# Performance work log

Hardware: AMD Instinct MI355X
Metric: run time of the kernel (lower is better)

## Reference

```python
import jax, jax.numpy as jnp
import numpy as np

SMOOTHING = 0.9  # NEURON_CONFIG['signal_smoothing']
NUM_SOURCE = 16384
NUM_TARGET = 16384
NUM_BRANCHES = 64
BATCH = 32


def setup_inputs() -> dict:
    key = jax.random.key(0)
    k1, k2, k3, k4 = jax.random.split(key, 4)
    spikes = jax.random.normal(k1, (BATCH, NUM_SOURCE), dtype=jnp.float32)
    attenuation = jax.random.uniform(k2, (NUM_SOURCE, NUM_BRANCHES), dtype=jnp.float32)
    target_indices = jax.random.randint(k3, (NUM_SOURCE, NUM_BRANCHES), 0, NUM_TARGET)
    delays = jax.random.randint(k4, (NUM_SOURCE, NUM_BRANCHES), 0, 6)
    return {"spikes": spikes, "attenuation": attenuation,
            "target_indices": target_indices, "delays": delays}


def reference(spikes, attenuation, target_indices, delays):
    # spikes: [B, S]; attenuation/delays/target_indices: [S, Br]
    B = spikes.shape[0]
    num_target = NUM_TARGET
    att = jnp.clip(attenuation, 0.0, 1.0)
    decay = SMOOTHING ** delays.astype(spikes.dtype)          # [S, Br]
    # fused elementwise: signal per (batch, source, branch)
    signals = spikes[:, :, None] * (att * decay)[None, :, :]   # [B, S, Br]
    flat_t = target_indices.reshape(-1)                        # [S*Br]
    flat_s = signals.reshape(B, -1)                            # [B, S*Br]
    out = jnp.zeros((B, num_target), dtype=spikes.dtype)
    out = out.at[jnp.arange(B)[:, None], flat_t[None, :]].add(flat_s)
    return out
```

## Files before the change

kernel.cpp:

```cpp
#include <hip/hip_runtime.h>

#define S_   16384
#define T_   16384
#define B_   32
#define NEDGES (S_ * 64)
#define GP_  512
#define EPG  2048
#define NBKT 256
#define TPB  64
#define CAPT 128
#define OVF_CAP 64

__device__ __forceinline__ float edge_weight(float a, int d) {
  float w = fminf(fmaxf(a, 0.0f), 1.0f);
  float r = (d & 1) ? 0.9f : 1.0f;
  r = (d & 2) ? r * 0.81f   : r;
  r = (d & 4) ? r * 0.6561f : r;
  return w * r;
}

__global__ __launch_bounds__(512) void produce(
    const float* __restrict__ spikes,
    const float* __restrict__ att,
    const int*   __restrict__ tgt,
    const int*   __restrict__ del,
    float*        __restrict__ spikesT,
    int2*         __restrict__ rec,
    unsigned int* __restrict__ ofse) {
  __shared__ float tile[32][33];
  __shared__ int4  sbuf4[EPG / 2];
  __shared__ int   cnt5[NBKT], cur5[NBKT], sofs5[NBKT];
  __shared__ int   wtot[4];
  int2* buf = (int2*)sbuf4;

  const int g   = blockIdx.x;
  const int tid = threadIdx.x;
  if (tid < NBKT) cnt5[tid] = 0;

  const int s0 = g * 32;
  {
    const int x = tid & 31, y = tid >> 5;
    tile[x][y]      = spikes[(size_t)y        * S_ + s0 + x];
    tile[x][y + 16] = spikes[(size_t)(y + 16) * S_ + s0 + x];
  }

  const int e4  = g * 512 + tid;
  int4   t = reinterpret_cast<const int4*>(tgt)[e4];
  float4 a = reinterpret_cast<const float4*>(att)[e4];
  int4   d = reinterpret_cast<const int4*>(del)[e4];
  const int src = e4 >> 4;

  __syncthreads();

  {
    const int b = tid & 31, j = tid >> 5;
    spikesT[(size_t)(s0 + j)      * 32 + b] = tile[j][b];
    spikesT[(size_t)(s0 + j + 16) * 32 + b] = tile[j + 16][b];
  }

  const int bk0 = t.x >> 6, bk1 = t.y >> 6, bk2 = t.z >> 6, bk3 = t.w >> 6;
  __hip_atomic_fetch_add(&cnt5[bk0], 1, __ATOMIC_RELAXED, __HIP_MEMORY_SCOPE_WORKGROUP);
  __hip_atomic_fetch_add(&cnt5[bk1], 1, __ATOMIC_RELAXED, __HIP_MEMORY_SCOPE_WORKGROUP);
  __hip_atomic_fetch_add(&cnt5[bk2], 1, __ATOMIC_RELAXED, __HIP_MEMORY_SCOPE_WORKGROUP);
  __hip_atomic_fetch_add(&cnt5[bk3], 1, __ATOMIC_RELAXED, __HIP_MEMORY_SCOPE_WORKGROUP);
  __syncthreads();

  int v = 0, incl = 0;
  if (tid < NBKT) {
    v = cnt5[tid];
    incl = v;
#pragma unroll
    for (int off = 1; off < 64; off <<= 1) {
      int u = __shfl_up(incl, off);
      if ((tid & 63) >= off) incl += u;
    }
    if ((tid & 63) == 63) wtot[tid >> 6] = incl;
  }
  __syncthreads();
  if (tid < NBKT) {
    int base = 0;
    const int wv = tid >> 6;
    for (int i = 0; i < wv; ++i) base += wtot[i];
    const int start = base + incl - v;
    sofs5[tid] = start;
    cur5[tid]  = start;
  }
  __syncthreads();

#define PUT(BK, TL, AV, DV)                                                   \
  {                                                                           \
    int p = __hip_atomic_fetch_add(&cur5[BK], 1, __ATOMIC_RELAXED,            \
                                   __HIP_MEMORY_SCOPE_WORKGROUP);             \
    buf[p] = make_int2(((TL) << 14) | src,                                    \
                       __float_as_int(edge_weight((AV), (DV))));              \
  }
  PUT(bk0, t.x & 63, a.x, d.x)
  PUT(bk1, t.y & 63, a.y, d.y)
  PUT(bk2, t.z & 63, a.z, d.z)
  PUT(bk3, t.w & 63, a.w, d.w)
#undef PUT
  __syncthreads();

  int4* recO = reinterpret_cast<int4*>(rec) + (size_t)g * (EPG / 2);
  recO[tid]       = sbuf4[tid];
  recO[tid + 512] = sbuf4[tid + 512];
  if (tid < NBKT)
    ofse[(size_t)tid * GP_ + g] =
        ((unsigned)cur5[tid] << 16) | (unsigned)sofs5[tid];
}

__global__ __launch_bounds__(1024) void consume(
    const int2*  __restrict__ rec,
    const unsigned int* __restrict__ ofse,
    const float* __restrict__ spikesT,
    float* __restrict__ out) {
  __shared__ int2  srt[TPB * CAPT];
  __shared__ float otile[TPB][33];
  __shared__ unsigned sse[GP_];
  __shared__ int   cur64[TPB];
  __shared__ int2  ovf[OVF_CAP];
  __shared__ int   ovfn;

  const int k   = blockIdx.x;
  const int tid = threadIdx.x;
  const int b   = tid & 31;
  const int hw  = tid >> 5;

  if (tid < TPB) cur64[tid] = tid * CAPT;
  if (tid == 0)  ovfn = 0;
  if (tid < GP_) sse[tid] = ofse[(size_t)k * GP_ + tid];
  __syncthreads();

  {
    const int grp = tid >> 3;
    const int l8  = tid & 7;
    for (int it = 0; it < 4; ++it) {
      const int g = grp + it * 128;
      const unsigned u = sse[g];
      const int st = (int)(u & 0xFFFF);
      const int n  = (int)(u >> 16) - st;
      const int2* slice = rec + (size_t)g * EPG + st;
      for (int j = l8; j < n; j += 8) {
        int2 r = slice[j];
        const int tl = (r.x >> 14) & 63;
        int p = __hip_atomic_fetch_add(&cur64[tl], 1, __ATOMIC_RELAXED,
                                       __HIP_MEMORY_SCOPE_WORKGROUP);
        if (p < (tl + 1) * CAPT) {
          srt[p] = r;
        } else {
          int q = __hip_atomic_fetch_add(&ovfn, 1, __ATOMIC_RELAXED,
                                         __HIP_MEMORY_SCOPE_WORKGROUP);
          if (q < OVF_CAP) ovf[q] = r;
        }
      }
    }
  }
  __syncthreads();

  float acc0 = 0.f, acc1 = 0.f;
  int e0 = hw * CAPT;
  int e1 = (hw + 32) * CAPT;
  const int e0e = min(cur64[hw],      (hw + 1)  * CAPT);
  const int e1e = min(cur64[hw + 32], (hw + 33) * CAPT);

  for (; e0 + 4 <= e0e && e1 + 4 <= e1e; e0 += 4, e1 += 4) {
    int2 r0 = srt[e0], r1 = srt[e0 + 1], r2 = srt[e0 + 2], r3 = srt[e0 + 3];
    int2 q0 = srt[e1], q1 = srt[e1 + 1], q2 = srt[e1 + 2], q3 = srt[e1 + 3];
    float s0 = spikesT[(size_t)(r0.x & 0x3FFF) * 32 + b];
    float s1 = spikesT[(size_t)(r1.x & 0x3FFF) * 32 + b];
    float s2 = spikesT[(size_t)(r2.x & 0x3FFF) * 32 + b];
    float s3 = spikesT[(size_t)(r3.x & 0x3FFF) * 32 + b];
    float u0 = spikesT[(size_t)(q0.x & 0x3FFF) * 32 + b];
    float u1 = spikesT[(size_t)(q1.x & 0x3FFF) * 32 + b];
    float u2 = spikesT[(size_t)(q2.x & 0x3FFF) * 32 + b];
    float u3 = spikesT[(size_t)(q3.x & 0x3FFF) * 32 + b];
    acc0 = fmaf(__int_as_float(r0.y), s0, acc0);
    acc0 = fmaf(__int_as_float(r1.y), s1, acc0);
    acc0 = fmaf(__int_as_float(r2.y), s2, acc0);
    acc0 = fmaf(__int_as_float(r3.y), s3, acc0);
    acc1 = fmaf(__int_as_float(q0.y), u0, acc1);
    acc1 = fmaf(__int_as_float(q1.y), u1, acc1);
    acc1 = fmaf(__int_as_float(q2.y), u2, acc1);
    acc1 = fmaf(__int_as_float(q3.y), u3, acc1);
  }
  for (; e0 + 4 <= e0e; e0 += 4) {
    int2 r0 = srt[e0], r1 = srt[e0 + 1], r2 = srt[e0 + 2], r3 = srt[e0 + 3];
    float s0 = spikesT[(size_t)(r0.x & 0x3FFF) * 32 + b];
    float s1 = spikesT[(size_t)(r1.x & 0x3FFF) * 32 + b];
    float s2 = spikesT[(size_t)(r2.x & 0x3FFF) * 32 + b];
    float s3 = spikesT[(size_t)(r3.x & 0x3FFF) * 32 + b];
    acc0 = fmaf(__int_as_float(r0.y), s0, acc0);
    acc0 = fmaf(__int_as_float(r1.y), s1, acc0);
    acc0 = fmaf(__int_as_float(r2.y), s2, acc0);
    acc0 = fmaf(__int_as_float(r3.y), s3, acc0);
  }
  for (; e0 < e0e; ++e0) {
    int2 r = srt[e0];
    acc0 = fmaf(__int_as_float(r.y), spikesT[(size_t)(r.x & 0x3FFF) * 32 + b], acc0);
  }
  for (; e1 + 4 <= e1e; e1 += 4) {
    int2 q0 = srt[e1], q1 = srt[e1 + 1], q2 = srt[e1 + 2], q3 = srt[e1 + 3];
    float u0 = spikesT[(size_t)(q0.x & 0x3FFF) * 32 + b];
    float u1 = spikesT[(size_t)(q1.x & 0x3FFF) * 32 + b];
    float u2 = spikesT[(size_t)(q2.x & 0x3FFF) * 32 + b];
    float u3 = spikesT[(size_t)(q3.x & 0x3FFF) * 32 + b];
    acc1 = fmaf(__int_as_float(q0.y), u0, acc1);
    acc1 = fmaf(__int_as_float(q1.y), u1, acc1);
    acc1 = fmaf(__int_as_float(q2.y), u2, acc1);
    acc1 = fmaf(__int_as_float(q3.y), u3, acc1);
  }
  for (; e1 < e1e; ++e1) {
    int2 q = srt[e1];
    acc1 = fmaf(__int_as_float(q.y), spikesT[(size_t)(q.x & 0x3FFF) * 32 + b], acc1);
  }

  const int no = min(ovfn, OVF_CAP);
  for (int j = 0; j < no; ++j) {
    int2 r = ovf[j];
    const int tl = (r.x >> 14) & 63;
    float s = spikesT[(size_t)(r.x & 0x3FFF) * 32 + b];
    float w = __int_as_float(r.y);
    if (tl == hw)      acc0 = fmaf(w, s, acc0);
    if (tl == hw + 32) acc1 = fmaf(w, s, acc1);
  }

  otile[hw][b]      = acc0;
  otile[hw + 32][b] = acc1;
  __syncthreads();
  const int bb = tid >> 5;
  const int cc = (tid & 31) * 2;
  float2 o2 = make_float2(otile[cc][bb], otile[cc + 1][bb]);
  *reinterpret_cast<float2*>(&out[(size_t)bb * T_ + k * 64 + cc]) = o2;
}

__global__ void zero_floats(float* __restrict__ p, int n) {
  int i = blockIdx.x * blockDim.x + threadIdx.x;
  if (i < n) p[i] = 0.0f;
}

__global__ void naive_kernel(const float* __restrict__ spikes,
                             const float* __restrict__ att,
                             const int*   __restrict__ tgt,
                             const int*   __restrict__ del,
                             float*       __restrict__ out) {
  int i = blockIdx.x * blockDim.x + threadIdx.x;
  if (i >= NEDGES) return;
  int   s = i >> 6;
  int   t = tgt[i];
  float w = edge_weight(att[i], del[i]);
  for (int b = 0; b < B_; ++b)
    unsafeAtomicAdd(&out[(size_t)b * T_ + t], w * spikes[(size_t)b * S_ + s]);
}

extern "C" void kernel_launch(void* const* d_in, const int* in_sizes, int n_in,
                              void* d_out, int out_size, void* d_ws, size_t ws_size,
                              hipStream_t stream) {
  const float* spikes = (const float*)d_in[0];
  const float* att    = (const float*)d_in[1];
  const int*   tgt    = (const int*)d_in[2];
  const int*   del    = (const int*)d_in[3];
  float*       out    = (float*)d_out;

  const size_t spikesT_bytes = (size_t)S_ * B_ * sizeof(float);
  const size_t rec_bytes     = (size_t)NEDGES * sizeof(int2);
  const size_t ofse_bytes    = (size_t)GP_ * NBKT * sizeof(unsigned);
  const size_t need = spikesT_bytes + rec_bytes + ofse_bytes + 64;

  if (ws_size < need) {
    zero_floats<<<(B_ * T_ + 255) / 256, 256, 0, stream>>>(out, B_ * T_);
    naive_kernel<<<(NEDGES + 255) / 256, 256, 0, stream>>>(spikes, att, tgt, del, out);
    return;
  }

  char* p = (char*)d_ws;
  float*        spikesT = (float*)p;        p += spikesT_bytes;
  int2*         rec     = (int2*)p;         p += rec_bytes;
  unsigned int* ofse    = (unsigned int*)p;

  produce<<<GP_, 512, 0, stream>>>(spikes, att, tgt, del, spikesT, rec, ofse);
  consume<<<NBKT, 1024, 0, stream>>>(rec, ofse, spikesT, out);
}
```

Before: 87.70 us.

## Scatter edges directly into per-bucket global regions via global atomic cursors

Instead of staging each producer block's edges in shared memory and writing a per-block bucket offset table, the producer reserves space with one global atomic per bucket and writes records straight into a contiguous per-bucket region, with a small global overflow list. The consumer then streams its bucket's records with vectorized contiguous loads instead of walking 512 small per-group slices. This removes the LDS staging, the prefix scan and the fragmented consumer reads. In exchange it adds a memset launch, global atomics, scattered 8-byte global writes from the producer, and a serial single-thread scan of the overflow list.

New measurement: 102.1 us. 16.4% more time.

```diff
diff --git a/kernel.cpp b/kernel.cpp
--- a/kernel.cpp
+++ b/kernel.cpp
@@ -10,6 +10,8 @@
 #define TPB  64
 #define CAPT 128
 #define OVF_CAP 64
+#define REG  5120
+#define GOVF_CAP 1024
 
 __device__ __forceinline__ float edge_weight(float a, int d) {
   float w = fminf(fmaxf(a, 0.0f), 1.0f);
@@ -26,16 +28,14 @@
     const int*   __restrict__ del,
     float*        __restrict__ spikesT,
     int2*         __restrict__ rec,
-    unsigned int* __restrict__ ofse) {
+    unsigned int* __restrict__ gcur,
+    int2*         __restrict__ govf) {
   __shared__ float tile[32][33];
-  __shared__ int4  sbuf4[EPG / 2];
-  __shared__ int   cnt5[NBKT], cur5[NBKT], sofs5[NBKT];
-  __shared__ int   wtot[4];
-  int2* buf = (int2*)sbuf4;
+  __shared__ int   cnt5[NBKT], cur5[NBKT], base5[NBKT];
 
   const int g   = blockIdx.x;
   const int tid = threadIdx.x;
-  if (tid < NBKT) cnt5[tid] = 0;
+  if (tid < NBKT) { cnt5[tid] = 0; cur5[tid] = 0; }
 
   const int s0 = g * 32;
   {
@@ -65,61 +65,47 @@
   __hip_atomic_fetch_add(&cnt5[bk3], 1, __ATOMIC_RELAXED, __HIP_MEMORY_SCOPE_WORKGROUP);
   __syncthreads();
 
-  int v = 0, incl = 0;
-  if (tid < NBKT) {
-    v = cnt5[tid];
-    incl = v;
-#pragma unroll
-    for (int off = 1; off < 64; off <<= 1) {
-      int u = __shfl_up(incl, off);
-      if ((tid & 63) >= off) incl += u;
-    }
-    if ((tid & 63) == 63) wtot[tid >> 6] = incl;
-  }
-  __syncthreads();
-  if (tid < NBKT) {
-    int base = 0;
-    const int wv = tid >> 6;
-    for (int i = 0; i < wv; ++i) base += wtot[i];
-    const int start = base + incl - v;
-    sofs5[tid] = start;
-    cur5[tid]  = start;
-  }
+  if (tid < NBKT)
+    base5[tid] = (int)__hip_atomic_fetch_add(&gcur[(size_t)tid * 16],
+                                             (unsigned)cnt5[tid],
+                                             __ATOMIC_RELAXED,
+                                             __HIP_MEMORY_SCOPE_AGENT);
   __syncthreads();
 
 #define PUT(BK, TL, AV, DV)                                                   \
   {                                                                           \
     int p = __hip_atomic_fetch_add(&cur5[BK], 1, __ATOMIC_RELAXED,            \
                                    __HIP_MEMORY_SCOPE_WORKGROUP);             \
-    buf[p] = make_int2(((TL) << 14) | src,                                    \
-                       __float_as_int(edge_weight((AV), (DV))));              \
+    const int slot = base5[BK] + p;                                           \
+    const int wb = __float_as_int(edge_weight((AV), (DV)));                   \
+    if (slot < REG) {                                                         \
+      rec[(size_t)(BK) * REG + slot] = make_int2(((TL) << 14) | src, wb);     \
+    } else {                                                                  \
+      unsigned q = __hip_atomic_fetch_add(&gcur[(size_t)NBKT * 16], 1u,       \
+                                          __ATOMIC_RELAXED,                   \
+                                          __HIP_MEMORY_SCOPE_AGENT);          \
+      if (q < GOVF_CAP)                                                       \
+        govf[q] = make_int2(((BK) << 20) | ((TL) << 14) | src, wb);           \
+    }                                                                         \
   }
   PUT(bk0, t.x & 63, a.x, d.x)
   PUT(bk1, t.y & 63, a.y, d.y)
   PUT(bk2, t.z & 63, a.z, d.z)
   PUT(bk3, t.w & 63, a.w, d.w)
 #undef PUT
-  __syncthreads();
-
-  int4* recO = reinterpret_cast<int4*>(rec) + (size_t)g * (EPG / 2);
-  recO[tid]       = sbuf4[tid];
-  recO[tid + 512] = sbuf4[tid + 512];
-  if (tid < NBKT)
-    ofse[(size_t)tid * GP_ + g] =
-        ((unsigned)cur5[tid] << 16) | (unsigned)sofs5[tid];
 }
 
 __global__ __launch_bounds__(1024) void consume(
     const int2*  __restrict__ rec,
-    const unsigned int* __restrict__ ofse,
+    const unsigned int* __restrict__ gcur,
+    const int2*  __restrict__ govf,
     const float* __restrict__ spikesT,
     float* __restrict__ out) {
   __shared__ int2  srt[TPB * CAPT];
   __shared__ float otile[TPB][33];
-  __shared__ unsigned sse[GP_];
   __shared__ int   cur64[TPB];
-  __shared__ int2  ovf[OVF_CAP];
-  __shared__ int   ovfn;
+  __shared__ int2  lovf[OVF_CAP];
+  __shared__ int   lovfn;
 
   const int k   = blockIdx.x;
   const int tid = threadIdx.x;
@@ -127,34 +113,49 @@
   const int hw  = tid >> 5;
 
   if (tid < TPB) cur64[tid] = tid * CAPT;
-  if (tid == 0)  ovfn = 0;
-  if (tid < GP_) sse[tid] = ofse[(size_t)k * GP_ + tid];
-  __syncthreads();
-
+  if (tid == 0)  lovfn = 0;
+  __syncthreads();
+
+  const int n = min((int)gcur[(size_t)k * 16], REG);
+  const int2* myrec = rec + (size_t)k * REG;
+
+#define PLACE(R)                                                              \
+  {                                                                           \
+    const int tl_ = ((R).x >> 14) & 63;                                       \
+    int p_ = __hip_atomic_fetch_add(&cur64[tl_], 1, __ATOMIC_RELAXED,         \
+                                    __HIP_MEMORY_SCOPE_WORKGROUP);            \
+    if (p_ < (tl_ + 1) * CAPT) {                                              \
+      srt[p_] = (R);                                                          \
+    } else {                                                                  \
+      int q_ = __hip_atomic_fetch_add(&lovfn, 1, __ATOMIC_RELAXED,            \
+                                      __HIP_MEMORY_SCOPE_WORKGROUP);          \
+      if (q_ < OVF_CAP) lovf[q_] = (R);                                       \
+    }                                                                         \
+  }
+
+  for (int i0 = tid * 4; i0 + 4 <= n; i0 += 4096) {
+    const int4* p4 = reinterpret_cast<const int4*>(myrec + i0);
+    int4 x = p4[0], y = p4[1];
+    int2 r0 = make_int2(x.x, x.y), r1 = make_int2(x.z, x.w);
+    int2 r2 = make_int2(y.x, y.y), r3 = make_int2(y.z, y.w);
+    PLACE(r0) PLACE(r1) PLACE(r2) PLACE(r3)
+  }
   {
-    const int grp = tid >> 3;
-    const int l8  = tid & 7;
-    for (int it = 0; it < 4; ++it) {
-      const int g = grp + it * 128;
-      const unsigned u = sse[g];
-      const int st = (int)(u & 0xFFFF);
-      const int n  = (int)(u >> 16) - st;
-      const int2* slice = rec + (size_t)g * EPG + st;
-      for (int j = l8; j < n; j += 8) {
-        int2 r = slice[j];
-        const int tl = (r.x >> 14) & 63;
-        int p = __hip_atomic_fetch_add(&cur64[tl], 1, __ATOMIC_RELAXED,
-                                       __HIP_MEMORY_SCOPE_WORKGROUP);
-        if (p < (tl + 1) * CAPT) {
-          srt[p] = r;
-        } else {
-          int q = __hip_atomic_fetch_add(&ovfn, 1, __ATOMIC_RELAXED,
-                                         __HIP_MEMORY_SCOPE_WORKGROUP);
-          if (q < OVF_CAP) ovf[q] = r;
-        }
+    const int base = n & ~3;
+    const int idx  = base + tid;
+    if (idx < n) { int2 r = myrec[idx]; PLACE(r) }
+  }
+  if (tid == 0) {
+    int m = min((int)gcur[(size_t)NBKT * 16], GOVF_CAP);
+    for (int j = 0; j < m; ++j) {
+      int2 r = govf[j];
+      if (((r.x >> 20) & 0xFF) == k) {
+        int2 rr = make_int2(r.x & 0xFFFFF, r.y);
+        PLACE(rr)
       }
     }
   }
+#undef PLACE
   __syncthreads();
 
   float acc0 = 0.f, acc1 = 0.f;
@@ -214,9 +215,9 @@
     acc1 = fmaf(__int_as_float(q.y), spikesT[(size_t)(q.x & 0x3FFF) * 32 + b], acc1);
   }
 
-  const int no = min(ovfn, OVF_CAP);
+  const int no = min(lovfn, OVF_CAP);
   for (int j = 0; j < no; ++j) {
-    int2 r = ovf[j];
+    int2 r = lovf[j];
     const int tl = (r.x >> 14) & 63;
     float s = spikesT[(size_t)(r.x & 0x3FFF) * 32 + b];
     float w = __int_as_float(r.y);
@@ -262,9 +263,10 @@
   float*       out    = (float*)d_out;
 
   const size_t spikesT_bytes = (size_t)S_ * B_ * sizeof(float);
-  const size_t rec_bytes     = (size_t)NEDGES * sizeof(int2);
-  const size_t ofse_bytes    = (size_t)GP_ * NBKT * sizeof(unsigned);
-  const size_t need = spikesT_bytes + rec_bytes + ofse_bytes + 64;
+  const size_t rec_bytes     = (size_t)NBKT * REG * sizeof(int2);
+  const size_t gcur_bytes    = ((size_t)NBKT * 16 + 16) * sizeof(unsigned);
+  const size_t govf_bytes    = (size_t)GOVF_CAP * sizeof(int2);
+  const size_t need = spikesT_bytes + rec_bytes + gcur_bytes + govf_bytes + 64;
 
   if (ws_size < need) {
     zero_floats<<<(B_ * T_ + 255) / 256, 256, 0, stream>>>(out, B_ * T_);
@@ -275,8 +277,10 @@
   char* p = (char*)d_ws;
   float*        spikesT = (float*)p;        p += spikesT_bytes;
   int2*         rec     = (int2*)p;         p += rec_bytes;
-  unsigned int* ofse    = (unsigned int*)p;
-
-  produce<<<GP_, 512, 0, stream>>>(spikes, att, tgt, del, spikesT, rec, ofse);
-  consume<<<NBKT, 1024, 0, stream>>>(rec, ofse, spikesT, out);
-}
+  unsigned int* gcur    = (unsigned int*)p; p += gcur_bytes;
+  int2*         govf    = (int2*)p;
+
+  hipMemsetAsync(gcur, 0, gcur_bytes, stream);
+  produce<<<GP_, 512, 0, stream>>>(spikes, att, tgt, del, spikesT, rec, gcur, govf);
+  consume<<<NBKT, 1024, 0, stream>>>(rec, gcur, govf, spikesT, out);
+}
```
